# Kernel tuning notes

Hardware: AMD Instinct MI355X
Metric: run time of the kernel (lower is better)

## Reference

```python
import jax, jax.numpy as jnp
import numpy as np

B, S, H, I, E = 2, 2048, 1024, 4096, 8


def setup_inputs() -> dict:
    key = jax.random.key(0)
    k1, k2, k3, k4 = jax.random.split(key, 4)
    hidden_states = jax.random.normal(k1, (B, S, H), dtype=jnp.float32)
    # router: nn.Linear(H, E, bias=False) -> weight (E, H)
    Wr = jax.random.normal(k2, (E, H), dtype=jnp.float32) * 0.02
    # per-expert MLP: Linear(H,I) weight (I,H); Linear(I,H) weight (H,I); stacked over E
    W1 = jax.random.normal(k3, (E, I, H), dtype=jnp.float32) * 0.02
    W2 = jax.random.normal(k4, (E, H, I), dtype=jnp.float32) * 0.02
    return {"hidden_states": hidden_states, "Wr": Wr, "W1": W1, "W2": W2}


def reference(hidden_states, Wr, W1, W2):
    b, s, h = hidden_states.shape
    n_exp = Wr.shape[0]
    x = hidden_states.reshape(-1, h)                      # (N, H)
    logits = x @ Wr.T                                     # (N, E)
    probs = jax.nn.softmax(logits, axis=-1)               # (N, E)
    # top_k with k == num_experts: sorted probs descending (one-hot mask then
    # covers every expert, so each expert sees every token; expert i's output is
    # weighted by the i-th largest prob, exactly as the torch code does).
    top_probs, _ = jax.lax.top_k(probs, n_exp)            # (N, E)
    hmid = jnp.einsum('nh,eih->nei', x, W1)               # (N, E, I)
    hmid = jax.nn.gelu(hmid, approximate=False)           # exact erf GELU (torch nn.GELU default)
    yexp = jnp.einsum('nei,ehi->neh', hmid, W2)           # (N, E, H)
    out = jnp.einsum('neh,ne->nh', yexp, top_probs)       # weighted combine
    return out.reshape(b, s, h)
```

## Files before the change

kernel.cpp:

```cpp
#include <hip/hip_runtime.h>
#include <hip/hip_bf16.h>

#define NTOK 4096
#define HD   1024
#define ID   4096
#define NE   8

typedef float  floatx4 __attribute__((ext_vector_type(4)));
typedef __bf16 bf16x8  __attribute__((ext_vector_type(8)));
typedef unsigned short u16;

__device__ __forceinline__ u16 f2bf(float f) {
    union { float f; unsigned int i; } c; c.f = f;
    return (u16)((c.i + 0x7fffu + ((c.i >> 16) & 1u)) >> 16);
}

__device__ __forceinline__ void async_copy16(u16* lds, const u16* g) {
    __builtin_amdgcn_global_load_lds(
        (const __attribute__((address_space(1))) void*)g,
        (__attribute__((address_space(3))) void*)lds, 16, 0, 0);
}

__device__ __forceinline__ float gelu_fast(float v) {
    const float u = v * (0.7978845608f + 0.0356774081f * v * v);
    const float t = 1.f - 2.f / (__expf(2.f * u) + 1.f);
    return 0.5f * v * (1.f + t);
}

#define FENCE()  asm volatile("" ::: "memory")
#define BAR()    do { FENCE(); __builtin_amdgcn_s_barrier(); FENCE(); } while (0)
#define WAITV4() asm volatile("s_waitcnt vmcnt(4)" ::: "memory")
#define WAITV0() asm volatile("s_waitcnt vmcnt(0)" ::: "memory")
#define WAITL0() asm volatile("s_waitcnt lgkmcnt(0)" ::: "memory")

__global__ __launch_bounds__(256) void convert_kernel(
    const float* __restrict__ src, u16* __restrict__ dst)
{
    const size_t i = ((size_t)blockIdx.x * 256 + threadIdx.x) * 8;
    const float4 a = *(const float4*)(src + i);
    const float4 b = *(const float4*)(src + i + 4);
    ushort4 o0, o1;
    o0.x = f2bf(a.x); o0.y = f2bf(a.y); o0.z = f2bf(a.z); o0.w = f2bf(a.w);
    o1.x = f2bf(b.x); o1.y = f2bf(b.y); o1.z = f2bf(b.z); o1.w = f2bf(b.w);
    *(ushort4*)(dst + i)     = o0;
    *(ushort4*)(dst + i + 4) = o1;
}

__global__ __launch_bounds__(256) void convert2_kernel(
    const float* __restrict__ s1, u16* __restrict__ d1,
    const float* __restrict__ s2, u16* __restrict__ d2, int half)
{
    const int b = blockIdx.x;
    const float* src = (b < half) ? s1 : s2;
    u16*         dst = (b < half) ? d1 : d2;
    const int    bb  = (b < half) ? b : b - half;
    const size_t i = ((size_t)bb * 256 + threadIdx.x) * 8;
    const float4 a = *(const float4*)(src + i);
    const float4 c = *(const float4*)(src + i + 4);
    ushort4 o0, o1;
    o0.x = f2bf(a.x); o0.y = f2bf(a.y); o0.z = f2bf(a.z); o0.w = f2bf(a.w);
    o1.x = f2bf(c.x); o1.y = f2bf(c.y); o1.z = f2bf(c.z); o1.w = f2bf(c.w);
    *(ushort4*)(dst + i)     = o0;
    *(ushort4*)(dst + i + 4) = o1;
}

__global__ __launch_bounds__(256) void router_kernel(
    const float* __restrict__ x, const float* __restrict__ Wr,
    float* __restrict__ wbuf)
{
    const int n    = blockIdx.x * 4 + (threadIdx.x >> 6);
    const int lane = threadIdx.x & 63;
    const float* xr = x + (size_t)n * HD;
    float acc[NE];
#pragma unroll
    for (int e = 0; e < NE; ++e) acc[e] = 0.f;
    for (int h = lane; h < HD; h += 64) {
        const float xv = xr[h];
#pragma unroll
        for (int e = 0; e < NE; ++e) acc[e] += xv * Wr[e * HD + h];
    }
#pragma unroll
    for (int e = 0; e < NE; ++e) {
        float v = acc[e];
#pragma unroll
        for (int off = 32; off > 0; off >>= 1) v += __shfl_xor(v, off, 64);
        acc[e] = v;
    }
    float mx = acc[0];
#pragma unroll
    for (int e = 1; e < NE; ++e) mx = fmaxf(mx, acc[e]);
    float s = 0.f;
#pragma unroll
    for (int e = 0; e < NE; ++e) { acc[e] = __expf(acc[e] - mx); s += acc[e]; }
    const float inv = 1.f / s;
#pragma unroll
    for (int e = 0; e < NE; ++e) acc[e] *= inv;
#pragma unroll
    for (int i = 0; i < NE - 1; ++i)
#pragma unroll
        for (int j = 0; j < NE - 1 - i; ++j) {
            const float a = acc[j], b = acc[j + 1];
            acc[j] = fmaxf(a, b); acc[j + 1] = fminf(a, b);
        }
    if (lane < NE) wbuf[lane * NTOK + n] = acc[lane];
}

__device__ __forceinline__ void gemm256_tile(
    const u16* __restrict__ A, const u16* __restrict__ B,
    int ldA, int ldB, int K, int rowBase, int colBase,
    u16* As0, u16* As1, u16* Bs0, u16* Bs1,
    floatx4 acc[8][4])
{
    const int t    = threadIdx.x;
    const int w    = t >> 6, lane = t & 63;
    const int wm   = w & 1, wn = w >> 1;
    const int quad = lane >> 4, l15 = lane & 15;

    const int srow   = (w << 4) + (lane >> 2);
    const int schunk = ((lane & 3) ^ ((lane >> 3) & 3)) << 3;
    const u16* gA = A + (size_t)(rowBase + srow) * ldA + schunk;
    const u16* gB = B + (size_t)(colBase + srow) * ldB + schunk;
    const size_t hA = (size_t)128 * ldA, hB = (size_t)128 * ldB;
    u16* lA0 = As0 + w * 512;
    u16* lA1 = As1 + w * 512;
    u16* lB0 = Bs0 + w * 512;
    u16* lB1 = Bs1 + w * 512;

    const int sw = (l15 >> 1) & 3;
    int aoff[8], boff[4];
#pragma unroll
    for (int mi = 0; mi < 8; ++mi)
        aoff[mi] = (wm * 128 + mi * 16 + l15) * 32 + ((quad ^ sw) << 3);
#pragma unroll
    for (int ni = 0; ni < 4; ++ni)
        boff[ni] = (wn * 64 + ni * 16 + l15) * 32 + ((quad ^ sw) << 3);

#define STAGE2(lA, lB, kt) do { const int _ko = (kt) << 5;          \
        async_copy16(lA,        gA + _ko);                          \
        async_copy16(lA + 4096, gA + _ko + hA);                     \
        async_copy16(lB,        gB + _ko);                          \
        async_copy16(lB + 4096, gB + _ko + hB); } while (0)

    const int nkt = K >> 5;
    bf16x8 af[8], bfr[4];
    STAGE2(lA0, lB0, 0);
    STAGE2(lA1, lB1, 1);

#pragma unroll 1
    for (int kt = 0; kt < nkt; kt += 2) {
        WAITV4(); BAR();
#pragma unroll
        for (int ni = 0; ni < 4; ++ni) bfr[ni] = *(const bf16x8*)(Bs0 + boff[ni]);
#pragma unroll
        for (int mi = 0; mi < 8; ++mi) af[mi] = *(const bf16x8*)(As0 + aoff[mi]);
        __builtin_amdgcn_s_setprio(1);
#pragma unroll
        for (int mi = 0; mi < 4; ++mi)
#pragma unroll
            for (int ni = 0; ni < 4; ++ni)
                acc[mi][ni] = __builtin_amdgcn_mfma_f32_16x16x32_bf16(
                    af[mi], bfr[ni], acc[mi][ni], 0, 0, 0);
        __builtin_amdgcn_s_setprio(0);
        WAITL0();
        BAR();
        if (kt + 2 < nkt) STAGE2(lA0, lB0, kt + 2);
        __builtin_amdgcn_s_setprio(1);
#pragma unroll
        for (int mi = 4; mi < 8; ++mi)
#pragma unroll
            for (int ni = 0; ni < 4; ++ni)
                acc[mi][ni] = __builtin_amdgcn_mfma_f32_16x16x32_bf16(
                    af[mi], bfr[ni], acc[mi][ni], 0, 0, 0);
        __builtin_amdgcn_s_setprio(0);
        if (kt + 2 < nkt) { WAITV4(); } else { WAITV0(); }
        BAR();
#pragma unroll
        for (int ni = 0; ni < 4; ++ni) bfr[ni] = *(const bf16x8*)(Bs1 + boff[ni]);
#pragma unroll
        for (int mi = 0; mi < 8; ++mi) af[mi] = *(const bf16x8*)(As1 + aoff[mi]);
        __builtin_amdgcn_s_setprio(1);
#pragma unroll
        for (int mi = 0; mi < 4; ++mi)
#pragma unroll
            for (int ni = 0; ni < 4; ++ni)
                acc[mi][ni] = __builtin_amdgcn_mfma_f32_16x16x32_bf16(
                    af[mi], bfr[ni], acc[mi][ni], 0, 0, 0);
        __builtin_amdgcn_s_setprio(0);
        WAITL0();
        BAR();
        if (kt + 3 < nkt) STAGE2(lA1, lB1, kt + 3);
        __builtin_amdgcn_s_setprio(1);
#pragma unroll
        for (int mi = 4; mi < 8; ++mi)
#pragma unroll
            for (int ni = 0; ni < 4; ++ni)
                acc[mi][ni] = __builtin_amdgcn_mfma_f32_16x16x32_bf16(
                    af[mi], bfr[ni], acc[mi][ni], 0, 0, 0);
        __builtin_amdgcn_s_setprio(0);
    }
#undef STAGE2
}

__global__ __launch_bounds__(512, 2) void gemm1_kernel(
    const u16* __restrict__ X, const u16* __restrict__ W1b,
    const float* __restrict__ wbuf, u16* __restrict__ hmid)
{
    __shared__ __align__(16) u16 As[2][8192];
    __shared__ __align__(16) u16 Bs[2][8192];
    floatx4 acc[8][4] = {};
    const int bid = blockIdx.x;
    const int x   = bid & 7;
    const int j   = bid >> 3;
    const int sub = j >> 7;
    const int nt  = x * 16 + sub * 8 + (j & 7);
    const int mt  = (j >> 3) & 15;
    const int rowBase = mt * 256, colBase = nt * 256;
    const int e  = colBase >> 12;
    const int ic0 = colBase & (ID - 1);

    gemm256_tile(X, W1b, HD, HD, HD, rowBase, colBase,
                 As[0], As[1], Bs[0], Bs[1], acc);

    u16* hm = hmid + (size_t)e * NTOK * ID;
    const int t = threadIdx.x, w = t >> 6, lane = t & 63;
    const int wm = w & 1, wn = w >> 1, quad = lane >> 4, l15 = lane & 15;
#pragma unroll
    for (int mi = 0; mi < 8; ++mi)
#pragma unroll
        for (int r = 0; r < 4; ++r) {
            const int row = rowBase + wm * 128 + mi * 16 + quad * 4 + r;
            const float wv = wbuf[e * NTOK + row];
#pragma unroll
            for (int ni = 0; ni < 4; ++ni) {
                const int ic = ic0 + wn * 64 + ni * 16 + l15;
                hm[(size_t)row * ID + ic] =
                    f2bf(gelu_fast(acc[mi][ni][r]) * wv);
            }
        }
}

__global__ __launch_bounds__(512, 2) void gemm2_kernel(
    const u16* __restrict__ hmid, const u16* __restrict__ W2b,
    float* __restrict__ acclo, float* __restrict__ acchi)
{
    __shared__ __align__(16) u16 As[2][8192];
    __shared__ __align__(16) u16 Bs[2][8192];
    floatx4 acc[8][4] = {};
    const int bid = blockIdx.x;
    const int swz = (bid & 7) * 64 + (bid >> 3);
    const int z = swz >> 6, mt = (swz >> 2) & 15, nt = swz & 3;
    const int rowBase = mt * 256, colBase = nt * 256;

    gemm256_tile(hmid + (size_t)z * NTOK * ID, W2b + (size_t)z * HD * ID,
                 ID, ID, ID, rowBase, colBase,
                 As[0], As[1], Bs[0], Bs[1], acc);

    const size_t NH = (size_t)NTOK * HD;
    float* accs = (z < 4) ? (acclo + (size_t)z * NH)
                          : (acchi + (size_t)(z - 4) * NH);
    const int t = threadIdx.x, w = t >> 6, lane = t & 63;
    const int wm = w & 1, wn = w >> 1, quad = lane >> 4, l15 = lane & 15;
#pragma unroll
    for (int mi = 0; mi < 8; ++mi)
#pragma unroll
        for (int r = 0; r < 4; ++r) {
            const int row = rowBase + wm * 128 + mi * 16 + quad * 4 + r;
#pragma unroll
            for (int ni = 0; ni < 4; ++ni) {
                const int col = colBase + wn * 64 + ni * 16 + l15;
                accs[(size_t)row * HD + col] = acc[mi][ni][r];
            }
        }
}

__global__ __launch_bounds__(256) void finalize_kernel(
    const float* __restrict__ acclo, const float* __restrict__ acchi,
    float* __restrict__ out)
{
    const size_t NH = (size_t)NTOK * HD;
    const size_t i = ((size_t)blockIdx.x * 256 + threadIdx.x) * 4;
    float4 o = *(const float4*)(acclo + i);
#pragma unroll
    for (int z = 1; z < 4; ++z) {
        const float4 a = *(const float4*)(acclo + (size_t)z * NH + i);
        o.x += a.x; o.y += a.y; o.z += a.z; o.w += a.w;
    }
#pragma unroll
    for (int z = 0; z < 4; ++z) {
        const float4 a = *(const float4*)(acchi + (size_t)z * NH + i);
        o.x += a.x; o.y += a.y; o.z += a.z; o.w += a.w;
    }
    *(float4*)(out + i) = o;
}

extern "C" void kernel_launch(void* const* d_in, const int* in_sizes, int n_in,
                              void* d_out, int out_size, void* d_ws, size_t ws_size,
                              hipStream_t stream) {
    const float* x  = (const float*)d_in[0];
    const float* Wr = (const float*)d_in[1];
    const float* W1 = (const float*)d_in[2];
    const float* W2 = (const float*)d_in[3];
    float* out = (float*)d_out;

    const size_t MB = 1024 * 1024;
    char* ws = (char*)d_ws;
    float* wbuf   = (float*)ws;
    u16*   Xb     = (u16*)(ws + 131072);
    u16*   W1b    = (u16*)(ws + 131072 + 8 * MB);
    u16*   W2b    = (u16*)(ws + 131072 + 72 * MB);
    u16*   hmid   = (u16*)(ws + 131072 + 136 * MB);
    float* acclo  = (float*)ws;
    float* acchi  = (float*)(ws + 131072 + 392 * MB);
    if (ws_size < 131072 + 456 * MB) return;

    convert_kernel<<<dim3((NTOK * HD) / 2048), 256, 0, stream>>>(x, Xb);
    convert2_kernel<<<dim3(2 * (NE * ID * HD) / 2048), 256, 0, stream>>>(
        W1, W1b, W2, W2b, (NE * ID * HD) / 2048);
    router_kernel<<<dim3(NTOK / 4), 256, 0, stream>>>(x, Wr, wbuf);

    gemm1_kernel<<<dim3(NE * ID / 256 * (NTOK / 256)), 512, 0, stream>>>(
        Xb, W1b, wbuf, hmid);
    gemm2_kernel<<<dim3((NTOK / 256) * (HD / 256) * 8), 512, 0, stream>>>(
        hmid, W2b, acclo, acchi);
    finalize_kernel<<<dim3(NTOK * HD / 1024), 256, 0, stream>>>(
        acclo, acchi, out);
}
```

Measured before the change: 946.3 us.

## Restructure GEMM main loop to single-barrier double buffering with interleaved LDS reads

Replaces the two-stage-in-flight prefetch loop, which had split barriers and waitcnt(vmcnt 4), with a simpler one-tile-ahead double buffer. Each iteration waits for all memory ops, hits one barrier, issues the next tile's async copy, then interleaves the A-fragment LDS reads with the MFMA groups. This halves the barriers per k-step and may lower register pressure, since fragments are read just before use. The cost is only one tile of global-load latency hidden, and a full vmcnt(0) wait each step could expose memory latency.

Result: slower. 1.084 ms (+14.5%).

```diff
diff --git a/kernel.cpp b/kernel.cpp
--- a/kernel.cpp
+++ b/kernel.cpp
@@ -27,11 +27,9 @@
     return 0.5f * v * (1.f + t);
 }
 
-#define FENCE()  asm volatile("" ::: "memory")
-#define BAR()    do { FENCE(); __builtin_amdgcn_s_barrier(); FENCE(); } while (0)
-#define WAITV4() asm volatile("s_waitcnt vmcnt(4)" ::: "memory")
-#define WAITV0() asm volatile("s_waitcnt vmcnt(0)" ::: "memory")
-#define WAITL0() asm volatile("s_waitcnt lgkmcnt(0)" ::: "memory")
+#define FENCE()   asm volatile("" ::: "memory")
+#define BAR()     do { FENCE(); __builtin_amdgcn_s_barrier(); FENCE(); } while (0)
+#define WAITALL() asm volatile("s_waitcnt vmcnt(0) lgkmcnt(0)" ::: "memory")
 
 __global__ __launch_bounds__(256) void convert_kernel(
     const float* __restrict__ src, u16* __restrict__ dst)
@@ -141,64 +139,42 @@
         async_copy16(lB,        gB + _ko);                          \
         async_copy16(lB + 4096, gB + _ko + hB); } while (0)
 
+#define RD(P, o) (*(const bf16x8*)((P) + (o)))
+#define MM4(AF, m) do {                                                     \
+        __builtin_amdgcn_s_setprio(1);                                      \
+        acc[m][0] = __builtin_amdgcn_mfma_f32_16x16x32_bf16(AF, b0, acc[m][0], 0, 0, 0); \
+        acc[m][1] = __builtin_amdgcn_mfma_f32_16x16x32_bf16(AF, b1, acc[m][1], 0, 0, 0); \
+        acc[m][2] = __builtin_amdgcn_mfma_f32_16x16x32_bf16(AF, b2, acc[m][2], 0, 0, 0); \
+        acc[m][3] = __builtin_amdgcn_mfma_f32_16x16x32_bf16(AF, b3, acc[m][3], 0, 0, 0); \
+        __builtin_amdgcn_s_setprio(0); } while (0)
+
     const int nkt = K >> 5;
-    bf16x8 af[8], bfr[4];
     STAGE2(lA0, lB0, 0);
-    STAGE2(lA1, lB1, 1);
 
 #pragma unroll 1
-    for (int kt = 0; kt < nkt; kt += 2) {
-        WAITV4(); BAR();
-#pragma unroll
-        for (int ni = 0; ni < 4; ++ni) bfr[ni] = *(const bf16x8*)(Bs0 + boff[ni]);
-#pragma unroll
-        for (int mi = 0; mi < 8; ++mi) af[mi] = *(const bf16x8*)(As0 + aoff[mi]);
-        __builtin_amdgcn_s_setprio(1);
-#pragma unroll
-        for (int mi = 0; mi < 4; ++mi)
-#pragma unroll
-            for (int ni = 0; ni < 4; ++ni)
-                acc[mi][ni] = __builtin_amdgcn_mfma_f32_16x16x32_bf16(
-                    af[mi], bfr[ni], acc[mi][ni], 0, 0, 0);
-        __builtin_amdgcn_s_setprio(0);
-        WAITL0();
+    for (int kt = 0; kt < nkt; ++kt) {
+        const u16* Ab = (kt & 1) ? As1 : As0;
+        const u16* Bb = (kt & 1) ? Bs1 : Bs0;
+        u16* sA = (kt & 1) ? lA0 : lA1;
+        u16* sB = (kt & 1) ? lB0 : lB1;
+        WAITALL();
         BAR();
-        if (kt + 2 < nkt) STAGE2(lA0, lB0, kt + 2);
-        __builtin_amdgcn_s_setprio(1);
-#pragma unroll
-        for (int mi = 4; mi < 8; ++mi)
-#pragma unroll
-            for (int ni = 0; ni < 4; ++ni)
-                acc[mi][ni] = __builtin_amdgcn_mfma_f32_16x16x32_bf16(
-                    af[mi], bfr[ni], acc[mi][ni], 0, 0, 0);
-        __builtin_amdgcn_s_setprio(0);
-        if (kt + 2 < nkt) { WAITV4(); } else { WAITV0(); }
-        BAR();
-#pragma unroll
-        for (int ni = 0; ni < 4; ++ni) bfr[ni] = *(const bf16x8*)(Bs1 + boff[ni]);
-#pragma unroll
-        for (int mi = 0; mi < 8; ++mi) af[mi] = *(const bf16x8*)(As1 + aoff[mi]);
-        __builtin_amdgcn_s_setprio(1);
-#pragma unroll
-        for (int mi = 0; mi < 4; ++mi)
-#pragma unroll
-            for (int ni = 0; ni < 4; ++ni)
-                acc[mi][ni] = __builtin_amdgcn_mfma_f32_16x16x32_bf16(
-                    af[mi], bfr[ni], acc[mi][ni], 0, 0, 0);
-        __builtin_amdgcn_s_setprio(0);
-        WAITL0();
-        BAR();
-        if (kt + 3 < nkt) STAGE2(lA1, lB1, kt + 3);
-        __builtin_amdgcn_s_setprio(1);
-#pragma unroll
-        for (int mi = 4; mi < 8; ++mi)
-#pragma unroll
-            for (int ni = 0; ni < 4; ++ni)
-                acc[mi][ni] = __builtin_amdgcn_mfma_f32_16x16x32_bf16(
-                    af[mi], bfr[ni], acc[mi][ni], 0, 0, 0);
-        __builtin_amdgcn_s_setprio(0);
+        if (kt + 1 < nkt) STAGE2(sA, sB, kt + 1);
+        bf16x8 b0 = RD(Bb, boff[0]), b1 = RD(Bb, boff[1]);
+        bf16x8 b2 = RD(Bb, boff[2]), b3 = RD(Bb, boff[3]);
+        bf16x8 a0 = RD(Ab, aoff[0]), a1 = RD(Ab, aoff[1]);
+        bf16x8 a2 = RD(Ab, aoff[2]);  MM4(a0, 0);
+        bf16x8 a3 = RD(Ab, aoff[3]);  MM4(a1, 1);
+        bf16x8 a4 = RD(Ab, aoff[4]);  MM4(a2, 2);
+        bf16x8 a5 = RD(Ab, aoff[5]);  MM4(a3, 3);
+        bf16x8 a6 = RD(Ab, aoff[6]);  MM4(a4, 4);
+        bf16x8 a7 = RD(Ab, aoff[7]);  MM4(a5, 5);
+        MM4(a6, 6);
+        MM4(a7, 7);
     }
 #undef STAGE2
+#undef RD
+#undef MM4
 }
 
 __global__ __launch_bounds__(512, 2) void gemm1_kernel(
```
